# Kernel tuning notes

Hardware: AMD Instinct MI355X
Metric: run time of the kernel (lower is better)

The kernel has to match this reference:

```python
import jax, jax.numpy as jnp
import numpy as np

B, S = 2, 2048            # 2 sequences of 2048 tokens (flattened ragged batch)
H, KV, D = 32, 8, 128     # query heads, kv heads (GQA), head dim
DM = H * D                # 4096 model dim


def setup_inputs() -> dict:
    key = jax.random.key(0)
    k1, k2, k3 = jax.random.split(key, 3)
    T = B * S
    hidden_states = jax.random.normal(k1, (T, DM), dtype=jnp.float32)
    # Llama RoPE tables per token position (positions restart per sequence)
    pos = jnp.tile(jnp.arange(S, dtype=jnp.float32), B)            # [T]
    inv_freq = 1.0 / (10000.0 ** (jnp.arange(0, D, 2, dtype=jnp.float32) / D))  # [D/2]
    freqs = pos[:, None] * inv_freq[None, :]                       # [T, D/2]
    emb = jnp.concatenate([freqs, freqs], axis=-1)                 # [T, D]
    cos, sin = jnp.cos(emb), jnp.sin(emb)
    qkv_weight = jax.random.normal(k2, ((H + 2 * KV) * D, DM), dtype=jnp.float32) * (DM ** -0.5)
    o_weight = jax.random.normal(k3, (DM, DM), dtype=jnp.float32) * (DM ** -0.5)
    return {"hidden_states": hidden_states, "cos": cos, "sin": sin,
            "qkv_weight": qkv_weight, "o_weight": o_weight}


def _rotate_half(x):
    x1, x2 = jnp.split(x, 2, axis=-1)
    return jnp.concatenate([-x2, x1], axis=-1)


def reference(hidden_states, cos, sin, qkv_weight, o_weight):
    T = hidden_states.shape[0]
    # fused QKV projection (torch Linear: x @ W.T)
    qkv = hidden_states @ qkv_weight.T                  # [T, (H+2KV)*D]
    qkv = qkv.reshape(T, H + 2 * KV, D)
    q, k, v = jnp.split(qkv, [H, H + KV], axis=1)       # [T,H,D], [T,KV,D], [T,KV,D]
    # RoPE (rotate-half), cos/sin broadcast over heads
    c, s = cos[:, None, :], sin[:, None, :]
    q = q * c + _rotate_half(q) * s
    k = k * c + _rotate_half(k) * s
    # causal GQA attention per sequence
    qb = q.reshape(B, S, H, D)
    kb = jnp.repeat(k.reshape(B, S, KV, D), H // KV, axis=2)  # [B,S,H,D]
    vb = jnp.repeat(v.reshape(B, S, KV, D), H // KV, axis=2)
    scale = D ** -0.5
    scores = jnp.einsum('bqhd,bkhd->bhqk', qb, kb) * scale    # [B,H,S,S]
    causal = jnp.tril(jnp.ones((S, S), dtype=bool))
    scores = jnp.where(causal[None, None], scores, jnp.finfo(scores.dtype).min)
    attn = jax.nn.softmax(scores, axis=-1)
    out = jnp.einsum('bhqk,bkhd->bqhd', attn, vb)             # [B,S,H,D]
    out = out.reshape(1, T, H * D)
    return out @ o_weight.T                                    # [1, T, DM]
```

## Files before the change

kernel.cpp:

```cpp
#include <hip/hip_runtime.h>
#include <hip/hip_bf16.h>

#define TT   4096
#define DM   4096
#define NH   32
#define NKV  8
#define HD   128
#define SLEN 2048
#define NQKV 6144

typedef __bf16 bf16x4 __attribute__((ext_vector_type(4)));
typedef __bf16 bf16x8 __attribute__((ext_vector_type(8)));
typedef float  f32x4  __attribute__((ext_vector_type(4)));

#define GBM 128
#define GBN 128
#define GBK 64

template <typename CT>
__global__ __launch_bounds__(256) void mfma_gemm_nt(const float* __restrict__ A,
                                                    const float* __restrict__ B,
                                                    CT* __restrict__ C,
                                                    int M, int N, int K) {
    __shared__ __bf16 As[GBM * GBK];
    __shared__ __bf16 Bs[GBM * GBK];

    const int tid  = threadIdx.x;
    const int lane = tid & 63;

    const int nwg = gridDim.x * gridDim.y;
    const int bid = blockIdx.y * gridDim.x + blockIdx.x;
    const int cpx = nwg >> 3;
    const int swz = (bid & 7) * cpx + (bid >> 3);
    const int bx = swz % gridDim.x;
    const int by = swz / gridDim.x;

    const size_t bm = (size_t)by * GBM;
    const size_t bn = (size_t)bx * GBN;

    const int srow0 = tid >> 4;
    const int scol  = (tid & 15) << 2;

    const float* Ag = A + (bm + srow0) * (size_t)K + scol;
    const float* Bg = B + (bn + srow0) * (size_t)K + scol;

    f32x4 pa[8], pb[8];
#pragma unroll
    for (int i = 0; i < 8; ++i) {
        pa[i] = *(const f32x4*)(Ag + (size_t)(16 * i) * K);
        pb[i] = *(const f32x4*)(Bg + (size_t)(16 * i) * K);
    }

    f32x4 acc[4][4];
#pragma unroll
    for (int m = 0; m < 4; ++m)
#pragma unroll
        for (int n = 0; n < 4; ++n)
#pragma unroll
            for (int r = 0; r < 4; ++r) acc[m][n][r] = 0.f;

    const int wid  = tid >> 6;
    const int wr   = wid >> 1;
    const int wc   = wid & 1;
    const int lrow = lane & 15;
    const int lkhi = lane >> 4;

    char* AsB = (char*)As;
    char* BsB = (char*)Bs;

    const int nk = K / GBK;
    for (int kt = 0; kt < nk; ++kt) {
        __syncthreads();
#pragma unroll
        for (int i = 0; i < 8; ++i) {
            const int row = srow0 + 16 * i;
            bf16x4 wa, wb;
#pragma unroll
            for (int j = 0; j < 4; ++j) {
                wa[j] = (__bf16)pa[i][j];
                wb[j] = (__bf16)pb[i][j];
            }
            const int off = row * 128 + ((scol << 1) ^ ((row & 7) << 4));
            *(bf16x4*)(AsB + off) = wa;
            *(bf16x4*)(BsB + off) = wb;
        }
        __syncthreads();

        if (kt + 1 < nk) {
            Ag += GBK; Bg += GBK;
#pragma unroll
            for (int i = 0; i < 8; ++i) {
                pa[i] = *(const f32x4*)(Ag + (size_t)(16 * i) * K);
                pb[i] = *(const f32x4*)(Bg + (size_t)(16 * i) * K);
            }
        }

#pragma unroll
        for (int kk = 0; kk < 2; ++kk) {
            bf16x8 af[4], bfr[4];
#pragma unroll
            for (int m = 0; m < 4; ++m) {
                const int rowa = wr * 64 + m * 16 + lrow;
                af[m] = *(const bf16x8*)(AsB + rowa * 128 +
                         ((kk * 64 + lkhi * 16) ^ ((rowa & 7) << 4)));
                const int rowb = wc * 64 + m * 16 + lrow;
                bfr[m] = *(const bf16x8*)(BsB + rowb * 128 +
                         ((kk * 64 + lkhi * 16) ^ ((rowb & 7) << 4)));
            }
#pragma unroll
            for (int m = 0; m < 4; ++m)
#pragma unroll
                for (int n = 0; n < 4; ++n)
                    acc[m][n] = __builtin_amdgcn_mfma_f32_16x16x32_bf16(
                                    af[m], bfr[n], acc[m][n], 0, 0, 0);
        }
    }

    const int crow0 = wr * 64 + (lane >> 4) * 4;
    const int ccol0 = wc * 64 + (lane & 15);
#pragma unroll
    for (int m = 0; m < 4; ++m)
#pragma unroll
        for (int n = 0; n < 4; ++n) {
            CT* cp = C + (bm + crow0 + m * 16) * (size_t)N + bn + ccol0 + n * 16;
#pragma unroll
            for (int r = 0; r < 4; ++r)
                cp[(size_t)r * N] = (CT)acc[m][n][r];
        }
}

__global__ __launch_bounds__(256) void rope_bf16(__bf16* __restrict__ qkv,
                                                 const float* __restrict__ cosb,
                                                 const float* __restrict__ sinb) {
    int idx = blockIdx.x * blockDim.x + threadIdx.x;
    int dg = idx & 15;
    int h  = (idx >> 4) % 40;
    int t  = idx / (16 * 40);
    __bf16* row = qkv + (size_t)t * NQKV + h * HD;
    int d0 = dg * 4;
    bf16x4 x1 = *(bf16x4*)(row + d0);
    bf16x4 x2 = *(bf16x4*)(row + 64 + d0);
    f32x4 c = *(const f32x4*)(cosb + t * HD + d0);
    f32x4 s = *(const f32x4*)(sinb + t * HD + d0);
    bf16x4 o1, o2;
#pragma unroll
    for (int j = 0; j < 4; ++j) {
        float a = (float)x1[j], b = (float)x2[j];
        o1[j] = (__bf16)(a * c[j] - b * s[j]);
        o2[j] = (__bf16)(b * c[j] + a * s[j]);
    }
    *(bf16x4*)(row + d0) = o1;
    *(bf16x4*)(row + 64 + d0) = o2;
}

__global__ __launch_bounds__(256) void attn_mfma(const __bf16* __restrict__ qkv,
                                                 float* __restrict__ ctx) {
    __shared__ __bf16 Ks[64 * 128];
    __shared__ __bf16 Vt[128 * 64];
    __shared__ float  Ps[4 * 16 * 68];

    const int tid  = threadIdx.x;
    const int w    = tid >> 6;
    const int lane = tid & 63;
    const int lr   = lane & 15;
    const int lq   = lane >> 4;

    const int qt = gridDim.x - 1 - blockIdx.x;
    const int bh = blockIdx.y;
    const int b = bh >> 5, h = bh & 31, g = h >> 2;
    const int q0 = qt * 64;

    const __bf16* qrow = qkv + (size_t)(b * SLEN + q0 + w * 16 + lr) * NQKV + h * HD;
    bf16x8 qf[4];
#pragma unroll
    for (int kd = 0; kd < 4; ++kd)
        qf[kd] = *(const bf16x8*)(qrow + kd * 32 + lq * 8);

    f32x4 o[8];
    float m[4], l[4];
#pragma unroll
    for (int df = 0; df < 8; ++df)
#pragma unroll
        for (int r = 0; r < 4; ++r) o[df][r] = 0.f;
#pragma unroll
    for (int r = 0; r < 4; ++r) { m[r] = -3.0e38f; l[r] = 0.f; }

    char* KsB = (char*)Ks;
    char* VtB = (char*)Vt;
    float* Pw = Ps + w * 16 * 68;

    const int srow = tid >> 4;
    const int sch  = tid & 15;
    const __bf16* kglob = qkv + (size_t)(b * SLEN) * NQKV + (NH + g) * HD + sch * 8;
    const __bf16* vglob = qkv + (size_t)(b * SLEN) * NQKV + (NH + NKV + g) * HD + sch * 8;

    const float scale = 0.08838834764831845f;

    for (int kv0 = 0; kv0 <= q0; kv0 += 64) {
        __syncthreads();
#pragma unroll
        for (int p = 0; p < 4; ++p) {
            const int k = p * 16 + srow;
            bf16x8 k8 = *(const bf16x8*)(kglob + (size_t)(kv0 + k) * NQKV);
            *(bf16x8*)(KsB + k * 256 + ((sch * 16) ^ ((k & 15) * 16))) = k8;
            bf16x8 v8 = *(const bf16x8*)(vglob + (size_t)(kv0 + k) * NQKV);
            const int d0 = sch * 8;
#pragma unroll
            for (int e = 0; e < 8; ++e) {
                const int d = d0 + e;
                *(__bf16*)(VtB + d * 128 + ((k * 2) ^ (((d >> 1) & 7) << 4))) = v8[e];
            }
        }
        __syncthreads();

        f32x4 sacc[4];
#pragma unroll
        for (int n = 0; n < 4; ++n)
#pragma unroll
            for (int r = 0; r < 4; ++r) sacc[n][r] = 0.f;
#pragma unroll
        for (int kd = 0; kd < 4; ++kd) {
#pragma unroll
            for (int n = 0; n < 4; ++n) {
                const int row = n * 16 + lr;
                bf16x8 kf = *(const bf16x8*)(KsB + row * 256 +
                              (((kd * 4 + lq) * 16) ^ (lr * 16)));
                sacc[n] = __builtin_amdgcn_mfma_f32_16x16x32_bf16(
                              qf[kd], kf, sacc[n], 0, 0, 0);
            }
        }

        float pv[4][4];
        float tm[4] = {-3.0e38f, -3.0e38f, -3.0e38f, -3.0e38f};
#pragma unroll
        for (int n = 0; n < 4; ++n)
#pragma unroll
            for (int r = 0; r < 4; ++r) {
                const int qi = q0 + w * 16 + lq * 4 + r;
                const int ki = kv0 + lr + 16 * n;
                const float s = (ki <= qi) ? sacc[n][r] * scale : -3.0e38f;
                pv[n][r] = s;
                tm[r] = fmaxf(tm[r], s);
            }
#pragma unroll
        for (int r = 0; r < 4; ++r) {
            tm[r] = fmaxf(tm[r], __shfl_xor(tm[r], 1));
            tm[r] = fmaxf(tm[r], __shfl_xor(tm[r], 2));
            tm[r] = fmaxf(tm[r], __shfl_xor(tm[r], 4));
            tm[r] = fmaxf(tm[r], __shfl_xor(tm[r], 8));
            const float mn = fmaxf(m[r], tm[r]);
            const float al = __expf(m[r] - mn);
            m[r] = mn;
            float t = 0.f;
#pragma unroll
            for (int n = 0; n < 4; ++n) {
                const float p = __expf(pv[n][r] - mn);
                pv[n][r] = p;
                t += p;
            }
            t += __shfl_xor(t, 1);
            t += __shfl_xor(t, 2);
            t += __shfl_xor(t, 4);
            t += __shfl_xor(t, 8);
            l[r] = l[r] * al + t;
#pragma unroll
            for (int df = 0; df < 8; ++df) o[df][r] *= al;
#pragma unroll
            for (int n = 0; n < 4; ++n)
                Pw[(lq * 4 + r) * 68 + lr + 16 * n] = pv[n][r];
        }

#pragma unroll
        for (int ks = 0; ks < 2; ++ks) {
            float a8[8];
            *(f32x4*)&a8[0] = *(const f32x4*)&Pw[lr * 68 + ks * 32 + lq * 8];
            *(f32x4*)&a8[4] = *(const f32x4*)&Pw[lr * 68 + ks * 32 + lq * 8 + 4];
            bf16x8 af;
#pragma unroll
            for (int e = 0; e < 8; ++e) af[e] = (__bf16)a8[e];
#pragma unroll
            for (int df = 0; df < 8; ++df) {
                const int d = df * 16 + lr;
                bf16x8 vf = *(const bf16x8*)(VtB + d * 128 +
                              (((ks * 4 + lq) * 16) ^ (((d >> 1) & 7) << 4)));
                o[df] = __builtin_amdgcn_mfma_f32_16x16x32_bf16(af, vf, o[df], 0, 0, 0);
            }
        }
    }

    float inv[4];
#pragma unroll
    for (int r = 0; r < 4; ++r) inv[r] = 1.0f / l[r];
#pragma unroll
    for (int df = 0; df < 8; ++df)
#pragma unroll
        for (int r = 0; r < 4; ++r) {
            const size_t row = (size_t)(b * SLEN + q0 + w * 16 + lq * 4 + r);
            ctx[row * DM + h * HD + df * 16 + lr] = o[df][r] * inv[r];
        }
}

extern "C" void kernel_launch(void* const* d_in, const int* in_sizes, int n_in,
                              void* d_out, int out_size, void* d_ws, size_t ws_size,
                              hipStream_t stream) {
    const float* hs   = (const float*)d_in[0];
    const float* cosb = (const float*)d_in[1];
    const float* sinb = (const float*)d_in[2];
    const float* wqkv = (const float*)d_in[3];
    const float* wo   = (const float*)d_in[4];
    float* out = (float*)d_out;

    __bf16* qkv = (__bf16*)d_ws;
    float*  ctx = (float*)((char*)d_ws + (size_t)TT * NQKV * 2);

    dim3 blk(256);

    mfma_gemm_nt<__bf16><<<dim3(NQKV / GBN, TT / GBM), blk, 0, stream>>>(
        hs, wqkv, qkv, TT, NQKV, DM);

    rope_bf16<<<(TT * 40 * 16) / 256, 256, 0, stream>>>(qkv, cosb, sinb);

    attn_mfma<<<dim3(SLEN / 64, 2 * NH), blk, 0, stream>>>(qkv, ctx);

    mfma_gemm_nt<float><<<dim3(DM / GBN, TT / GBM), blk, 0, stream>>>(
        ctx, wo, out, TT, DM, DM);
}
```

Baseline: 1.467 ms.

## Prefetch KV tiles into registers and keep softmax probabilities in registers

The attention kernel now loads the next K/V tile into registers while the current tile is computed, so global-load latency overlaps with MFMA work. QK^T is computed transposed, giving each lane one query column. Softmax row max and sum then reduce with two cross-lane shuffles instead of four per row. The P matrix moves into the PV MFMA operand layout through lane shuffles rather than a shared-memory round trip, and the V transpose writes packed pairs with a new swizzle instead of single bf16 stores. This raises register pressure and adds shuffle traffic in exchange for less LDS traffic and fewer synchronisation stalls.

```diff
diff --git a/kernel.cpp b/kernel.cpp
--- a/kernel.cpp
+++ b/kernel.cpp
@@ -9,9 +9,14 @@
 #define SLEN 2048
 #define NQKV 6144
 
+typedef __bf16 bf16x2 __attribute__((ext_vector_type(2)));
 typedef __bf16 bf16x4 __attribute__((ext_vector_type(4)));
 typedef __bf16 bf16x8 __attribute__((ext_vector_type(8)));
 typedef float  f32x4  __attribute__((ext_vector_type(4)));
+typedef unsigned int u32;
+typedef u32 u32x4 __attribute__((ext_vector_type(4)));
+
+#define VSWZ(d) ((((d) & 7) ^ (((d) >> 3) & 7)) << 4)
 
 #define GBM 128
 #define GBN 128
@@ -157,7 +162,6 @@
                                                  float* __restrict__ ctx) {
     __shared__ __bf16 Ks[64 * 128];
     __shared__ __bf16 Vt[128 * 64];
-    __shared__ float  Ps[4 * 16 * 68];
 
     const int tid  = threadIdx.x;
     const int w    = tid >> 6;
@@ -177,17 +181,14 @@
         qf[kd] = *(const bf16x8*)(qrow + kd * 32 + lq * 8);
 
     f32x4 o[8];
-    float m[4], l[4];
 #pragma unroll
     for (int df = 0; df < 8; ++df)
 #pragma unroll
         for (int r = 0; r < 4; ++r) o[df][r] = 0.f;
-#pragma unroll
-    for (int r = 0; r < 4; ++r) { m[r] = -3.0e38f; l[r] = 0.f; }
+    float m_ = -3.0e38f, l_ = 0.f;
 
     char* KsB = (char*)Ks;
     char* VtB = (char*)Vt;
-    float* Pw = Ps + w * 16 * 68;
 
     const int srow = tid >> 4;
     const int sch  = tid & 15;
@@ -195,20 +196,49 @@
     const __bf16* vglob = qkv + (size_t)(b * SLEN) * NQKV + (NH + NKV + g) * HD + sch * 8;
 
     const float scale = 0.08838834764831845f;
+    const int qi_ = q0 + w * 16 + lr;
+    const int sparity = srow & 1;
+
+    bf16x8 kreg[4], vreg[4];
+#pragma unroll
+    for (int p = 0; p < 4; ++p) {
+        kreg[p] = *(const bf16x8*)(kglob + (size_t)(p * 16 + srow) * NQKV);
+        vreg[p] = *(const bf16x8*)(vglob + (size_t)(p * 16 + srow) * NQKV);
+    }
 
     for (int kv0 = 0; kv0 <= q0; kv0 += 64) {
         __syncthreads();
 #pragma unroll
         for (int p = 0; p < 4; ++p) {
             const int k = p * 16 + srow;
-            bf16x8 k8 = *(const bf16x8*)(kglob + (size_t)(kv0 + k) * NQKV);
-            *(bf16x8*)(KsB + k * 256 + ((sch * 16) ^ ((k & 15) * 16))) = k8;
-            bf16x8 v8 = *(const bf16x8*)(vglob + (size_t)(kv0 + k) * NQKV);
-            const int d0 = sch * 8;
-#pragma unroll
-            for (int e = 0; e < 8; ++e) {
-                const int d = d0 + e;
-                *(__bf16*)(VtB + d * 128 + ((k * 2) ^ (((d >> 1) & 7) << 4))) = v8[e];
+            *(bf16x8*)(KsB + k * 256 + ((sch * 16) ^ ((k & 15) << 4))) = kreg[p];
+        }
+#pragma unroll
+        for (int p = 0; p < 4; ++p) {
+            const int k  = p * 16 + srow;
+            const int ke = k & ~1;
+            u32x4 mine = __builtin_bit_cast(u32x4, vreg[p]);
+            u32x4 part;
+#pragma unroll
+            for (int c = 0; c < 4; ++c) part[c] = __shfl_xor((int)mine[c], 16);
+            bf16x8 vm = __builtin_bit_cast(bf16x8, mine);
+            bf16x8 vp = __builtin_bit_cast(bf16x8, part);
+#pragma unroll
+            for (int jj = 0; jj < 4; ++jj) {
+                const int j = sparity * 4 + jj;
+                const int d = sch * 8 + j;
+                bf16x2 val;
+                val[0] = sparity ? vp[j] : vm[j];
+                val[1] = sparity ? vm[j] : vp[j];
+                *(u32*)(VtB + d * 128 + ((ke * 2) ^ VSWZ(d))) =
+                    __builtin_bit_cast(u32, val);
+            }
+        }
+        if (kv0 + 64 <= q0) {
+#pragma unroll
+            for (int p = 0; p < 4; ++p) {
+                kreg[p] = *(const bf16x8*)(kglob + (size_t)(kv0 + 64 + p * 16 + srow) * NQKV);
+                vreg[p] = *(const bf16x8*)(vglob + (size_t)(kv0 + 64 + p * 16 + srow) * NQKV);
             }
         }
         __syncthreads();
@@ -224,79 +254,103 @@
             for (int n = 0; n < 4; ++n) {
                 const int row = n * 16 + lr;
                 bf16x8 kf = *(const bf16x8*)(KsB + row * 256 +
-                              (((kd * 4 + lq) * 16) ^ (lr * 16)));
+                              (((kd * 4 + lq) * 16) ^ ((row & 15) << 4)));
                 sacc[n] = __builtin_amdgcn_mfma_f32_16x16x32_bf16(
-                              qf[kd], kf, sacc[n], 0, 0, 0);
-            }
-        }
-
-        float pv[4][4];
-        float tm[4] = {-3.0e38f, -3.0e38f, -3.0e38f, -3.0e38f};
+                              kf, qf[kd], sacc[n], 0, 0, 0);
+            }
+        }
+
+        float p_[4][4];
 #pragma unroll
         for (int n = 0; n < 4; ++n)
 #pragma unroll
             for (int r = 0; r < 4; ++r) {
-                const int qi = q0 + w * 16 + lq * 4 + r;
-                const int ki = kv0 + lr + 16 * n;
-                const float s = (ki <= qi) ? sacc[n][r] * scale : -3.0e38f;
-                pv[n][r] = s;
-                tm[r] = fmaxf(tm[r], s);
-            }
-#pragma unroll
-        for (int r = 0; r < 4; ++r) {
-            tm[r] = fmaxf(tm[r], __shfl_xor(tm[r], 1));
-            tm[r] = fmaxf(tm[r], __shfl_xor(tm[r], 2));
-            tm[r] = fmaxf(tm[r], __shfl_xor(tm[r], 4));
-            tm[r] = fmaxf(tm[r], __shfl_xor(tm[r], 8));
-            const float mn = fmaxf(m[r], tm[r]);
-            const float al = __expf(m[r] - mn);
-            m[r] = mn;
-            float t = 0.f;
-#pragma unroll
-            for (int n = 0; n < 4; ++n) {
-                const float p = __expf(pv[n][r] - mn);
-                pv[n][r] = p;
-                t += p;
-            }
-            t += __shfl_xor(t, 1);
-            t += __shfl_xor(t, 2);
-            t += __shfl_xor(t, 4);
-            t += __shfl_xor(t, 8);
-            l[r] = l[r] * al + t;
-#pragma unroll
-            for (int df = 0; df < 8; ++df) o[df][r] *= al;
-#pragma unroll
-            for (int n = 0; n < 4; ++n)
-                Pw[(lq * 4 + r) * 68 + lr + 16 * n] = pv[n][r];
-        }
+                const int ki = kv0 + 16 * n + lq * 4 + r;
+                p_[n][r] = (ki <= qi_) ? sacc[n][r] * scale : -3.0e38f;
+            }
+        float rm[4];
+#pragma unroll
+        for (int n = 0; n < 4; ++n)
+            rm[n] = fmaxf(fmaxf(p_[n][0], p_[n][1]), fmaxf(p_[n][2], p_[n][3]));
+        float tm = fmaxf(fmaxf(rm[0], rm[1]), fmaxf(rm[2], rm[3]));
+        tm = fmaxf(tm, __shfl_xor(tm, 16));
+        tm = fmaxf(tm, __shfl_xor(tm, 32));
+        const float mn = fmaxf(m_, tm);
+        const float al = __expf(m_ - mn);
+        m_ = mn;
+        float rs[4];
+#pragma unroll
+        for (int n = 0; n < 4; ++n) {
+#pragma unroll
+            for (int r = 0; r < 4; ++r) {
+                p_[n][r] = __expf(p_[n][r] - mn);
+            }
+            rs[n] = (p_[n][0] + p_[n][1]) + (p_[n][2] + p_[n][3]);
+        }
+        float ts = (rs[0] + rs[1]) + (rs[2] + rs[3]);
+        ts += __shfl_xor(ts, 16);
+        ts += __shfl_xor(ts, 32);
+        l_ = l_ * al + ts;
+
+        float alr[4];
+#pragma unroll
+        for (int r = 0; r < 4; ++r)
+            alr[r] = __shfl(al, (lane & 0x30) | (lq * 4 + r));
+#pragma unroll
+        for (int df = 0; df < 8; ++df)
+#pragma unroll
+            for (int r = 0; r < 4; ++r) o[df][r] *= alr[r];
+
+        u32 q32[4][2];
+#pragma unroll
+        for (int n = 0; n < 4; ++n)
+#pragma unroll
+            for (int j = 0; j < 2; ++j) {
+                bf16x2 t;
+                t[0] = (__bf16)p_[n][2 * j];
+                t[1] = (__bf16)p_[n][2 * j + 1];
+                q32[n][j] = __builtin_bit_cast(u32, t);
+            }
+        const int sA = (((2 * lq) & 3) << 4) | lr;
+        const int sB = (((2 * lq + 1) & 3) << 4) | lr;
+        const bool hi = (lq >> 1) != 0;
 
 #pragma unroll
         for (int ks = 0; ks < 2; ++ks) {
-            float a8[8];
-            *(f32x4*)&a8[0] = *(const f32x4*)&Pw[lr * 68 + ks * 32 + lq * 8];
-            *(f32x4*)&a8[4] = *(const f32x4*)&Pw[lr * 68 + ks * 32 + lq * 8 + 4];
-            bf16x8 af;
-#pragma unroll
-            for (int e = 0; e < 8; ++e) af[e] = (__bf16)a8[e];
+            const u32 a0  = __shfl((int)q32[2 * ks][0],     sA);
+            const u32 a0b = __shfl((int)q32[2 * ks + 1][0], sA);
+            const u32 a1  = __shfl((int)q32[2 * ks][1],     sA);
+            const u32 a1b = __shfl((int)q32[2 * ks + 1][1], sA);
+            const u32 b0  = __shfl((int)q32[2 * ks][0],     sB);
+            const u32 b0b = __shfl((int)q32[2 * ks + 1][0], sB);
+            const u32 b1  = __shfl((int)q32[2 * ks][1],     sB);
+            const u32 b1b = __shfl((int)q32[2 * ks + 1][1], sB);
+            u32x4 wv;
+            wv[0] = hi ? a0b : a0;
+            wv[1] = hi ? a1b : a1;
+            wv[2] = hi ? b0b : b0;
+            wv[3] = hi ? b1b : b1;
+            bf16x8 af = __builtin_bit_cast(bf16x8, wv);
 #pragma unroll
             for (int df = 0; df < 8; ++df) {
                 const int d = df * 16 + lr;
                 bf16x8 vf = *(const bf16x8*)(VtB + d * 128 +
-                              (((ks * 4 + lq) * 16) ^ (((d >> 1) & 7) << 4)));
+                              (((ks * 4 + lq) * 16) ^ VSWZ(d)));
                 o[df] = __builtin_amdgcn_mfma_f32_16x16x32_bf16(af, vf, o[df], 0, 0, 0);
             }
         }
     }
 
-    float inv[4];
-#pragma unroll
-    for (int r = 0; r < 4; ++r) inv[r] = 1.0f / l[r];
+    float linv[4];
+#pragma unroll
+    for (int r = 0; r < 4; ++r)
+        linv[r] = 1.0f / __shfl(l_, (lane & 0x30) | (lq * 4 + r));
 #pragma unroll
     for (int df = 0; df < 8; ++df)
 #pragma unroll
         for (int r = 0; r < 4; ++r) {
             const size_t row = (size_t)(b * SLEN + q0 + w * 16 + lq * 4 + r);
-            ctx[row * DM + h * HD + df * 16 + lr] = o[df][r] * inv[r];
+            ctx[row * DM + h * HD + df * 16 + lr] = o[df][r] * linv[r];
         }
 }
 
```

New measurement: 1.358 ms. -7.4%, faster.
